# Performance work log

Measured on AMD Instinct MI355X. Metric: run time of the kernel, lower is better.

The kernel has to match this reference:

```python
import jax, jax.numpy as jnp
import numpy as np

EMBED_DIM = 128
BATCH = 16384
HIST = 200


def setup_inputs() -> dict:
    key = jax.random.key(0)
    k1, k2, k3, k4 = jax.random.split(key, 4)
    target_embedding = jax.random.normal(k1, (BATCH, EMBED_DIM), dtype=jnp.float32)
    hist_embeddings = jax.random.normal(k2, (BATCH, HIST, EMBED_DIM), dtype=jnp.float32)
    # Dense(embedding_dim, relu): kernel [D, D], bias [D]
    W_kernel = jax.random.normal(k3, (EMBED_DIM, EMBED_DIM), dtype=jnp.float32) * (1.0 / np.sqrt(EMBED_DIM))
    W_bias = jnp.zeros((EMBED_DIM,), dtype=jnp.float32)
    # Dense(1): kernel [D, 1], bias [1]
    q_kernel = jax.random.normal(k4, (EMBED_DIM, 1), dtype=jnp.float32) * (1.0 / np.sqrt(EMBED_DIM))
    q_bias = jnp.zeros((1,), dtype=jnp.float32)
    return {
        "target_embedding": target_embedding,
        "hist_embeddings": hist_embeddings,
        "W_kernel": W_kernel,
        "W_bias": W_bias,
        "q_kernel": q_kernel,
        "q_bias": q_bias,
    }


def reference(target_embedding, hist_embeddings, W_kernel, W_bias, q_kernel, q_bias):
    # target: [B, D] -> [B, 1, D]; broadcast add with hist [B, T, D]
    x = target_embedding[:, None, :] + hist_embeddings            # [B, T, D]
    h = jax.nn.relu(jnp.einsum('btd,de->bte', x, W_kernel) + W_bias)  # [B, T, D]
    logits = jnp.einsum('btd,do->bto', h, q_kernel) + q_bias      # [B, T, 1]
    scores = jax.nn.softmax(logits, axis=1)                       # [B, T, 1]
    return jnp.sum(scores * hist_embeddings, axis=1)              # [B, D]
```

## Files before the change

### kernel.cpp

```cpp
#include <hip/hip_runtime.h>
#include <hip/hip_bf16.h>

#define D_EMB 128
#define T_HIST 200
#define T_PAD 208
#define NG 6400
#define ITERS 32
#define NBLK 512

typedef float f32x4 __attribute__((ext_vector_type(4)));
typedef short bf16x8 __attribute__((ext_vector_type(8)));

__device__ __forceinline__ short f2bf(float f) {
    unsigned u = __builtin_bit_cast(unsigned, f);
    u += 0x7fffu + ((u >> 16) & 1u);
    return (short)(u >> 16);
}

__device__ __forceinline__ float dpp_reduce16(float x) {
    int v = __builtin_bit_cast(int, x);
    x += __builtin_bit_cast(float, __builtin_amdgcn_update_dpp(0, v, 0xB1, 0xF, 0xF, true));
    v = __builtin_bit_cast(int, x);
    x += __builtin_bit_cast(float, __builtin_amdgcn_update_dpp(0, v, 0x4E, 0xF, 0xF, true));
    v = __builtin_bit_cast(int, x);
    x += __builtin_bit_cast(float, __builtin_amdgcn_update_dpp(0, v, 0x141, 0xF, 0xF, true));
    v = __builtin_bit_cast(int, x);
    x += __builtin_bit_cast(float, __builtin_amdgcn_update_dpp(0, v, 0x140, 0xF, 0xF, true));
    return x;
}

__device__ __forceinline__ uint2 cvt_granule(f32x4 v) {
    uint2 r;
    asm("v_cvt_pk_bf16_f32 %0, %1, %2" : "=v"(r.x) : "v"(v[0]), "v"(v[1]));
    asm("v_cvt_pk_bf16_f32 %0, %1, %2" : "=v"(r.y) : "v"(v[2]), "v"(v[3]));
    return r;
}

__global__ void pack_w_kernel(const float* __restrict__ W, short* __restrict__ wfrag) {
    int tid = blockIdx.x * blockDim.x + threadIdx.x;
    int fragid = tid >> 6;
    int lane = tid & 63;
    int ks = fragid >> 3;
    int nt = fragid & 7;
    int n = nt * 16 + (lane & 15);
    int k0 = ks * 32 + (lane >> 4) * 8;
    bf16x8 r;
#pragma unroll
    for (int j = 0; j < 8; ++j) r[j] = f2bf(W[(k0 + j) * D_EMB + n]);
    ((bf16x8*)wfrag)[fragid * 64 + lane] = r;
}

__global__ void tw_kernel(const float* __restrict__ target, const float* __restrict__ W,
                          const float* __restrict__ bias, float* __restrict__ TW) {
    int e = threadIdx.x;
    int b0 = blockIdx.x * 8;
    float bv = bias[e];
    float acc[8];
#pragma unroll
    for (int i = 0; i < 8; ++i) acc[i] = bv;
    for (int d = 0; d < D_EMB; ++d) {
        float wv = W[d * D_EMB + e];
#pragma unroll
        for (int i = 0; i < 8; ++i)
            acc[i] = fmaf(target[(size_t)(b0 + i) * D_EMB + d], wv, acc[i]);
    }
#pragma unroll
    for (int i = 0; i < 8; ++i) TW[(size_t)(b0 + i) * D_EMB + e] = acc[i];
}

__launch_bounds__(512, 4)
__global__ void attn_main(const float* __restrict__ hist,
                          const float* __restrict__ TW,
                          const float* __restrict__ q,
                          const short* __restrict__ wfrag,
                          float* __restrict__ out) {
    __shared__ __align__(16) uint2 h2[T_PAD * 32];
    __shared__ float s_tw[D_EMB];
    __shared__ float s_logits[8][T_PAD];
    __shared__ float s_scores[T_PAD];
    __shared__ float s_red[16];
    __shared__ float s_p2[16][D_EMB];

    const int tid = threadIdx.x;
    const int l = tid & 63;
    const int w = tid >> 6;
    const int l15 = l & 15;
    const int lg = l >> 4;
    const int r = tid >> 5;
    const int cc = tid & 31;
    const int c_log = (((cc >> 1) ^ (r & 7)) << 1) | (cc & 1);
    const int base_g = r * 32 + c_log;
    const f32x4 vzero = {0.f, 0.f, 0.f, 0.f};

    bf16x8 Bf[4];
#pragma unroll
    for (int ks = 0; ks < 4; ++ks)
        Bf[ks] = ((const bf16x8*)wfrag)[(ks * 8 + w) * 64 + l];

    const float qv = q[w * 16 + l15];

    if (tid >= 256) h2[6144 + tid] = uint2{0u, 0u};

    const int base = blockIdx.x * ITERS;
    const f32x4* ghist = (const f32x4*)hist;

    f32x4 stg[13];
    float twstg = 0.f;

    {
        const f32x4* g0 = ghist + (size_t)base * NG;
#pragma unroll
        for (int k = 0; k < 12; ++k) stg[k] = g0[base_g + k * 512];
        if (tid < 256) stg[12] = g0[base_g + 12 * 512];
        if (tid < 128) twstg = TW[(size_t)base * D_EMB + tid];
    }

    for (int i = 0; i < ITERS; ++i) {
        const int b = base + i;

#pragma unroll
        for (int k = 0; k < 12; ++k) h2[tid + k * 512] = cvt_granule(stg[k]);
        if (tid < 256) h2[tid + 12 * 512] = cvt_granule(stg[12]);
        if (tid < 128) s_tw[tid] = twstg;
        __syncthreads();

        const float twv = s_tw[w * 16 + l15];
        const bf16x8* hp = (const bf16x8*)h2;
        for (int mt = 0; mt < 13; ++mt) {
            f32x4 acc = vzero;
#pragma unroll
            for (int ks = 0; ks < 4; ++ks) {
                bf16x8 A = hp[l15 * 16 + ((ks * 4 + lg) ^ (l15 & 7)) + mt * 256];
                acc = __builtin_amdgcn_mfma_f32_16x16x32_bf16(A, Bf[ks], acc, 0, 0, 0);
            }
            float part[4];
#pragma unroll
            for (int rr = 0; rr < 4; ++rr)
                part[rr] = fmaxf(acc[rr] + twv, 0.f) * qv;
#pragma unroll
            for (int rr = 0; rr < 4; ++rr) part[rr] = dpp_reduce16(part[rr]);
            if (l15 == 0) {
                int row = mt * 16 + lg * 4;
                f32x4 v;
#pragma unroll
                for (int rr = 0; rr < 4; ++rr)
                    v[rr] = (row + rr < T_HIST) ? part[rr] : -1e30f;
                *(f32x4*)&s_logits[w][row] = v;
            }
        }
        __syncthreads();

        float lv = -1e30f;
        if (tid < T_PAD) {
            lv = s_logits[0][tid] + s_logits[1][tid] + s_logits[2][tid] + s_logits[3][tid]
               + s_logits[4][tid] + s_logits[5][tid] + s_logits[6][tid] + s_logits[7][tid];
        }
        float m = lv;
#pragma unroll
        for (int off = 32; off >= 1; off >>= 1)
            m = fmaxf(m, __shfl_xor(m, off, 64));
        if (l == 0) s_red[w] = m;
        __syncthreads();
        float M = s_red[0];
#pragma unroll
        for (int k = 1; k < 8; ++k) M = fmaxf(M, s_red[k]);
        float e = (tid < T_PAD) ? __expf(lv - M) : 0.f;
        if (tid < T_PAD) s_scores[tid] = e;
        float sm = e;
#pragma unroll
        for (int off = 32; off >= 1; off >>= 1)
            sm += __shfl_xor(sm, off, 64);
        if (l == 0) s_red[8 + w] = sm;
        __syncthreads();
        float S = s_red[8];
#pragma unroll
        for (int k = 9; k < 16; ++k) S += s_red[k];

        f32x4 acc2 = vzero;
#pragma unroll
        for (int k = 0; k < 12; ++k) {
            float sc = s_scores[r + 16 * k];
#pragma unroll
            for (int rr = 0; rr < 4; ++rr)
                acc2[rr] = fmaf(sc, stg[k][rr], acc2[rr]);
        }
        if (tid < 256) {
            float sc = s_scores[r + 192];
#pragma unroll
            for (int rr = 0; rr < 4; ++rr)
                acc2[rr] = fmaf(sc, stg[12][rr], acc2[rr]);
        }
        *(f32x4*)&s_p2[r][c_log * 4] = acc2;
        __syncthreads();
        if (tid < 128) {
            float o = 0.f;
#pragma unroll
            for (int k = 0; k < 16; ++k) o += s_p2[k][tid];
            out[(size_t)b * D_EMB + tid] = o / S;
        }

        if (i + 1 < ITERS) {
            const f32x4* gn = ghist + (size_t)(b + 1) * NG;
#pragma unroll
            for (int k = 0; k < 12; ++k) stg[k] = gn[base_g + k * 512];
            if (tid < 256) stg[12] = gn[base_g + 12 * 512];
            if (tid < 128) twstg = TW[(size_t)(b + 1) * D_EMB + tid];
        }
    }
}

extern "C" void kernel_launch(void* const* d_in, const int* in_sizes, int n_in,
                              void* d_out, int out_size, void* d_ws, size_t ws_size,
                              hipStream_t stream) {
    const float* target = (const float*)d_in[0];
    const float* hist   = (const float*)d_in[1];
    const float* Wk     = (const float*)d_in[2];
    const float* Wb     = (const float*)d_in[3];
    const float* qk     = (const float*)d_in[4];
    float* out = (float*)d_out;

    short* wfrag = (short*)d_ws;
    float* TW    = (float*)((char*)d_ws + 32768);

    pack_w_kernel<<<dim3(8), dim3(256), 0, stream>>>(Wk, wfrag);
    tw_kernel<<<dim3(2048), dim3(128), 0, stream>>>(target, Wk, Wb, TW);
    attn_main<<<dim3(NBLK), dim3(512), 0, stream>>>(hist, TW, qk, wfrag, out);
}
```

Baseline: 387.2 us.

## Split history tile into two halves to overlap second-half loads with MFMA

Each batch's history tile is split into two halves held in separate LDS buffers. The second half's global loads are issued after the first half is converted, so they overlap the MFMA work on the first half, and only the first half is prefetched across iterations. Half of the blocks also sleep at start to stagger their memory bursts. The cost is an extra barrier per iteration and less cross-iteration prefetch depth, since the second half is now loaded inside the iteration.

```diff
diff --git a/kernel.cpp b/kernel.cpp
--- a/kernel.cpp
+++ b/kernel.cpp
@@ -74,7 +74,8 @@
                           const float* __restrict__ q,
                           const short* __restrict__ wfrag,
                           float* __restrict__ out) {
-    __shared__ __align__(16) uint2 h2[T_PAD * 32];
+    __shared__ __align__(16) uint2 bufH0[3584];
+    __shared__ __align__(16) uint2 bufH1[3072];
     __shared__ float s_tw[D_EMB];
     __shared__ float s_logits[8][T_PAD];
     __shared__ float s_scores[T_PAD];
@@ -96,22 +97,22 @@
 #pragma unroll
     for (int ks = 0; ks < 4; ++ks)
         Bf[ks] = ((const bf16x8*)wfrag)[(ks * 8 + w) * 64 + l];
-
     const float qv = q[w * 16 + l15];
 
-    if (tid >= 256) h2[6144 + tid] = uint2{0u, 0u};
+    if (tid >= 256) bufH1[2560 + tid] = uint2{0u, 0u};
+
+    if (blockIdx.x & 256) __builtin_amdgcn_s_sleep(120);
 
     const int base = blockIdx.x * ITERS;
     const f32x4* ghist = (const f32x4*)hist;
 
-    f32x4 stg[13];
+    f32x4 sH0[7], sH1[6];
     float twstg = 0.f;
 
     {
         const f32x4* g0 = ghist + (size_t)base * NG;
 #pragma unroll
-        for (int k = 0; k < 12; ++k) stg[k] = g0[base_g + k * 512];
-        if (tid < 256) stg[12] = g0[base_g + 12 * 512];
+        for (int k = 0; k < 7; ++k) sH0[k] = g0[base_g + k * 512];
         if (tid < 128) twstg = TW[(size_t)base * D_EMB + tid];
     }
 
@@ -119,18 +120,52 @@
         const int b = base + i;
 
 #pragma unroll
-        for (int k = 0; k < 12; ++k) h2[tid + k * 512] = cvt_granule(stg[k]);
-        if (tid < 256) h2[tid + 12 * 512] = cvt_granule(stg[12]);
+        for (int k = 0; k < 7; ++k) bufH0[tid + k * 512] = cvt_granule(sH0[k]);
         if (tid < 128) s_tw[tid] = twstg;
         __syncthreads();
 
+        {
+            const f32x4* g1 = ghist + (size_t)b * NG;
+#pragma unroll
+            for (int k = 0; k < 5; ++k) sH1[k] = g1[base_g + (7 + k) * 512];
+            if (tid < 256) sH1[5] = g1[base_g + 12 * 512];
+        }
+
         const float twv = s_tw[w * 16 + l15];
-        const bf16x8* hp = (const bf16x8*)h2;
-        for (int mt = 0; mt < 13; ++mt) {
+        const bf16x8* hp0 = (const bf16x8*)bufH0;
+        const bf16x8* hp1 = (const bf16x8*)bufH1;
+
+        for (int mt = 0; mt < 7; ++mt) {
             f32x4 acc = vzero;
 #pragma unroll
             for (int ks = 0; ks < 4; ++ks) {
-                bf16x8 A = hp[l15 * 16 + ((ks * 4 + lg) ^ (l15 & 7)) + mt * 256];
+                bf16x8 A = hp0[l15 * 16 + ((ks * 4 + lg) ^ (l15 & 7)) + mt * 256];
+                acc = __builtin_amdgcn_mfma_f32_16x16x32_bf16(A, Bf[ks], acc, 0, 0, 0);
+            }
+            float part[4];
+#pragma unroll
+            for (int rr = 0; rr < 4; ++rr)
+                part[rr] = fmaxf(acc[rr] + twv, 0.f) * qv;
+#pragma unroll
+            for (int rr = 0; rr < 4; ++rr) part[rr] = dpp_reduce16(part[rr]);
+            if (l15 == 0) {
+                f32x4 v;
+#pragma unroll
+                for (int rr = 0; rr < 4; ++rr) v[rr] = part[rr];
+                *(f32x4*)&s_logits[w][mt * 16 + lg * 4] = v;
+            }
+        }
+
+#pragma unroll
+        for (int k = 0; k < 5; ++k) bufH1[tid + k * 512] = cvt_granule(sH1[k]);
+        if (tid < 256) bufH1[tid + 5 * 512] = cvt_granule(sH1[5]);
+        __syncthreads();
+
+        for (int mt = 7; mt < 13; ++mt) {
+            f32x4 acc = vzero;
+#pragma unroll
+            for (int ks = 0; ks < 4; ++ks) {
+                bf16x8 A = hp1[l15 * 16 + ((ks * 4 + lg) ^ (l15 & 7)) + (mt - 7) * 256];
                 acc = __builtin_amdgcn_mfma_f32_16x16x32_bf16(A, Bf[ks], acc, 0, 0, 0);
             }
             float part[4];
@@ -178,17 +213,24 @@
 
         f32x4 acc2 = vzero;
 #pragma unroll
-        for (int k = 0; k < 12; ++k) {
+        for (int k = 0; k < 7; ++k) {
             float sc = s_scores[r + 16 * k];
 #pragma unroll
             for (int rr = 0; rr < 4; ++rr)
-                acc2[rr] = fmaf(sc, stg[k][rr], acc2[rr]);
+                acc2[rr] = fmaf(sc, sH0[k][rr], acc2[rr]);
+        }
+#pragma unroll
+        for (int k = 0; k < 5; ++k) {
+            float sc = s_scores[112 + r + 16 * k];
+#pragma unroll
+            for (int rr = 0; rr < 4; ++rr)
+                acc2[rr] = fmaf(sc, sH1[k][rr], acc2[rr]);
         }
         if (tid < 256) {
-            float sc = s_scores[r + 192];
-#pragma unroll
-            for (int rr = 0; rr < 4; ++rr)
-                acc2[rr] = fmaf(sc, stg[12][rr], acc2[rr]);
+            float sc = s_scores[192 + r];
+#pragma unroll
+            for (int rr = 0; rr < 4; ++rr)
+                acc2[rr] = fmaf(sc, sH1[5][rr], acc2[rr]);
         }
         *(f32x4*)&s_p2[r][c_log * 4] = acc2;
         __syncthreads();
@@ -202,8 +244,7 @@
         if (i + 1 < ITERS) {
             const f32x4* gn = ghist + (size_t)(b + 1) * NG;
 #pragma unroll
-            for (int k = 0; k < 12; ++k) stg[k] = gn[base_g + k * 512];
-            if (tid < 256) stg[12] = gn[base_g + 12 * 512];
+            for (int k = 0; k < 7; ++k) sH0[k] = gn[base_g + k * 512];
             if (tid < 128) twstg = TW[(size_t)(b + 1) * D_EMB + tid];
         }
     }
```

After: 365.6 us. 5.6% less time.
